# Optimization experiments

Measured on AMD Instinct MI355X. Metric: run time of the kernel, lower is better.

Reference implementation:

```python
import jax, jax.numpy as jnp
import numpy as np

JITTER = 0.05  # posterior-covariance jitter (constructor arg `jitter`)
TWO_PI = 2.0 * np.pi


def _local_k(x1, x2, ls, std):
    # 1-D RBF kernel: x1 (A,), x2 (B,) -> (A, B)
    d2 = jnp.square(x1[:, None] - x2[None, :])
    return (std * std) * jnp.exp(-0.5 * d2 / (ls * ls))


def setup_inputs() -> dict:
    key = jax.random.key(0)
    ks = jax.random.split(key, 8)
    N, D, M = 3072, 4, 512
    X = jax.random.normal(ks[0], (N, D), dtype=jnp.float32)
    y = jax.random.normal(ks[1], (N, 1), dtype=jnp.float32)
    X_bar = jax.random.normal(ks[2], (M, D), dtype=jnp.float32)
    # learned parameters (moderate positive values so fp32 Choleskys are stable)
    local_gp_ls = 1.0 + 0.1 * jax.random.normal(ks[3], (D,), dtype=jnp.float32)
    local_gp_std = 0.5 + 0.05 * jax.random.normal(ks[4], (D,), dtype=jnp.float32)
    local_gp_noise_std = 0.3 * jnp.ones((D,), dtype=jnp.float32)
    local_ls = 0.3 + 0.5 * jax.random.uniform(ks[5], (M, D), dtype=jnp.float32)
    global_gp_std = jnp.array([0.7], dtype=jnp.float32)
    global_gp_noise_std = jnp.array([0.5], dtype=jnp.float32)
    return {
        "X": X, "y": y, "X_bar": X_bar,
        "local_gp_ls": local_gp_ls, "local_gp_std": local_gp_std,
        "local_gp_noise_std": local_gp_noise_std, "local_ls": local_ls,
        "global_gp_std": global_gp_std, "global_gp_noise_std": global_gp_noise_std,
    }


def reference(X, y, X_bar, local_gp_ls, local_gp_std, local_gp_noise_std,
              local_ls, global_gp_std, global_gp_noise_std):
    # NSGP.nlml() in training mode.
    N, D = X.shape
    M = X_bar.shape[0]
    dtype = X.dtype
    eyeM = jnp.eye(M, dtype=dtype)
    eyeN = jnp.eye(N, dtype=dtype)
    log_lbar = jnp.log(jnp.abs(local_ls))  # (M, D)

    def per_dim(xb, xd, ls, std, noise, loglb):
        # local GP over inducing points for one input dimension
        k = _local_k(xb, xb, ls, std) + (noise * noise) * eyeM  # (M, M)
        c = jnp.linalg.cholesky(k)
        alpha = jax.scipy.linalg.cho_solve((c, True), loglb[:, None])  # (M, 1)
        kstar = _local_k(xd, xb, ls, std)  # (N, M)
        l = jnp.exp(kstar @ alpha)[:, 0]   # (N,) predicted lengthscales
        kss = _local_k(xd, xd, ls, std)    # (N, N)
        v = jax.scipy.linalg.cho_solve((c, True), kstar.T)  # (M, N)
        kpost = kss - kstar @ v + JITTER * eyeN             # posterior cov
        pc = jnp.linalg.cholesky(kpost)
        Bd = jnp.sum(jnp.log(jnp.diagonal(pc)))
        return l, Bd

    # batch the per-dimension local-GP work across the D input dims
    l_dn, B_d = jax.vmap(per_dim, in_axes=(1, 1, 0, 0, 0, 1))(
        X_bar, X, local_gp_ls, local_gp_std, local_gp_noise_std, log_lbar)
    l = l_dn.T  # (N, D)

    # nonstationary global kernel (Gibbs kernel)
    l1 = l[:, None, :]                    # (N, 1, D)
    l2 = l[None, :, :]                    # (1, N, D)
    lsq = l1 * l1 + l2 * l2               # (N, N, D)
    suffix = jnp.prod(jnp.sqrt(2.0 * l1 * l2 / lsq), axis=2)  # (N, N)
    d2 = jnp.square(X[:, None, :] - X[None, :, :])            # (N, N, D)
    gvar = global_gp_std[0] * global_gp_std[0]
    K = gvar * suffix * jnp.exp(-jnp.sum(d2 / lsq, axis=2))
    K = K + (global_gp_noise_std[0] ** 2) * eyeN

    L = jnp.linalg.cholesky(K)
    alpha = jax.scipy.linalg.cho_solve((L, True), y)  # (N, 1)
    log2pi = jnp.log(jnp.asarray(TWO_PI, dtype))
    A = 0.5 * ((y.T @ alpha)[0, 0]
               + jnp.sum(jnp.log(jnp.diagonal(L)))
               + N * log2pi)
    B = jnp.sum(B_d) + 0.5 * (M * D * log2pi)
    return A + B
```

## Files before the change

### kernel.cpp

```cpp
#include <hip/hip_runtime.h>
#include <math.h>

#define N_   3072
#define D_   4
#define M_   512
#define NPAD 3200
#define NB   128
#define PW   32
#define NBLK (NPAD/NB)
#define MBLK (M_/NB)
#define JITTER_ 0.05f
#define CBORD 32768.0f

__global__ __launch_bounds__(256)
void k_potrf_inv(float* Abase, size_t aStride, int lda, int kblk,
                 float* TinvBase, size_t tStride, int doInv,
                 float* logsum, int slotBase, int limit) {
  __shared__ float LT[NB*NB];
  __shared__ float Wp[10*PW*PW];
  __shared__ float Tt[3*PW*PW];
  __shared__ float pivd[NB];
  const int tid = threadIdx.x;
  float* A = Abase + (size_t)blockIdx.z * aStride;
  const int j0 = kblk * NB;

  for (int t = tid; t < NB*NB; t += 256) {
    int r = t & 127, c = t >> 7;
    LT[c*NB + r] = (c <= r) ? A[(size_t)(j0 + r)*lda + (j0 + c)] : 0.f;
  }
  __syncthreads();

  #pragma unroll
  for (int p = 0; p < 4; ++p) {
    const int pc0 = p*PW, pc1 = pc0 + PW;
    for (int j = pc0; j < pc1; ++j) {
      float d = fmaxf(LT[j*NB + j], 1e-30f);
      if (tid == 0) pivd[j] = d;
      float rd = 1.0f / d;
      int w = pc1 - 1 - j;
      for (int t = tid; t < w*NB; t += 256) {
        int c = j + 1 + (t >> 7);
        int i = t & 127;
        if (i >= c)
          LT[c*NB + i] -= LT[j*NB + i] * LT[j*NB + c] * rd;
      }
      __syncthreads();
    }
    for (int t = tid; t < PW*NB; t += 256) {
      int jc = pc0 + (t >> 7);
      int i  = t & 127;
      float dd = pivd[jc];
      if (i > jc)       LT[jc*NB + i] *= rsqrtf(dd);
      else if (i == jc) LT[jc*NB + i] = sqrtf(dd);
    }
    __syncthreads();
    if (pc1 < NB) {
      const int rem = NB - pc1;
      for (int t = tid; t < rem*rem; t += 256) {
        int cc = t / rem, rr = t - cc*rem;
        int c = pc1 + cc, i = pc1 + rr;
        if (i >= c) {
          float s = 0.f;
          #pragma unroll
          for (int jj = 0; jj < PW; ++jj)
            s += LT[(pc0+jj)*NB + i] * LT[(pc0+jj)*NB + c];
          LT[c*NB + i] -= s;
        }
      }
      __syncthreads();
    }
  }

  for (int t = tid; t < NB*NB; t += 256) {
    int r = t & 127, c = t >> 7;
    if (c <= r) A[(size_t)(j0 + r)*lda + (j0 + c)] = LT[c*NB + r];
  }
  {
    float lg = 0.f;
    if (tid < NB) {
      int g = j0 + tid;
      if (g < limit) lg = 0.5f * logf(pivd[tid]);
    }
    for (int o = 32; o; o >>= 1) lg += __shfl_down(lg, o);
    int wv = tid >> 6;
    if ((tid & 63) == 0 && wv < 2)
      logsum[(slotBase + blockIdx.z*32 + kblk)*2 + wv] = lg;
  }

  if (!doInv) return;

  for (int t = tid; t < 4*1024; t += 256) {
    int I = t >> 10, e = t & 1023;
    int r = e >> 5, c = e & 31;
    Wp[(I*(I+1)/2 + I)*1024 + e] = (r == c) ? 1.f : 0.f;
  }
  __syncthreads();
  {
    int wI = tid >> 6;
    int lane = tid & 63;
    float* Rb = &Wp[(wI*(wI+1)/2 + wI)*1024];
    for (int j = 0; j < 32; ++j) {
      float dinv = 1.0f / LT[(wI*32+j)*NB + (wI*32+j)];
      for (int t = lane; t < 1024; t += 64) {
        int i = t >> 5, c = t & 31;
        if (i > j && c <= j)
          Rb[i*32 + c] -= LT[(wI*32+j)*NB + (wI*32+i)] * Rb[j*32 + c] * dinv;
      }
      __syncthreads();
    }
    for (int t = lane; t < 1024; t += 64) {
      int i = t >> 5, c = t & 31;
      if (c <= i) Rb[t] *= 1.0f / LT[(wI*32+i)*NB + (wI*32+i)];
    }
    __syncthreads();
  }
  #pragma unroll
  for (int dist = 1; dist < 4; ++dist) {
    const int nb = 4 - dist;
    for (int t = tid; t < nb*1024; t += 256) {
      int b = t >> 10, e = t & 1023;
      int r = e >> 5, c = e & 31;
      int J = b, I = b + dist;
      float s = 0.f;
      for (int K = J; K < I; ++K) {
        const float* Wkj = &Wp[(K*(K+1)/2 + J)*1024];
        #pragma unroll
        for (int k = 0; k < 32; ++k)
          s += LT[(K*32+k)*NB + (I*32+r)] * Wkj[k*32 + c];
      }
      Tt[b*1024 + e] = s;
    }
    __syncthreads();
    for (int t = tid; t < nb*1024; t += 256) {
      int b = t >> 10, e = t & 1023;
      int r = e >> 5, c = e & 31;
      int J = b, I = b + dist;
      const float* Wii = &Wp[(I*(I+1)/2 + I)*1024];
      float s = 0.f;
      #pragma unroll
      for (int k = 0; k < 32; ++k)
        s += Wii[r*32 + k] * Tt[b*1024 + k*32 + c];
      Wp[(I*(I+1)/2 + J)*1024 + e] = -s;
    }
    __syncthreads();
  }
  {
    float* Tinv = TinvBase + (size_t)blockIdx.z * tStride;
    for (int t = tid; t < NB*32; t += 256) {
      int i = t >> 5, c4 = (t & 31) * 4;
      int I = i >> 5, J = c4 >> 5;
      float4 v;
      if (J <= I) {
        const float* Wij = &Wp[(I*(I+1)/2 + J)*1024 + (i & 31)*32 + (c4 & 31)];
        v = *(const float4*)Wij;
      } else v = make_float4(0.f, 0.f, 0.f, 0.f);
      *(float4*)&Tinv[i*NB + c4] = v;
    }
  }
}

__global__ __launch_bounds__(256)
void k_trsm(float* Abase, size_t aStride, int lda, int kblk,
            const float* TinvBase, size_t tStride) {
  __shared__ float As[32*68];
  __shared__ float Ts[32*132];
  const int tid = threadIdx.x;
  float* A = Abase + (size_t)blockIdx.z * aStride;
  const float* Tinv = TinvBase + (size_t)blockIdx.z * tStride;
  const int k0 = kblk * NB;
  const int row0 = k0 + NB + blockIdx.x * 64;
  const int tx = tid & 15, ty = tid >> 4;
  float acc[4][8];
  #pragma unroll
  for (int i = 0; i < 4; ++i)
    #pragma unroll
    for (int u = 0; u < 8; ++u) acc[i][u] = 0.f;
  for (int ks = 0; ks < NB; ks += 32) {
    for (int t = tid; t < 64*8; t += 256) {
      int r = t >> 3, q = t & 7;
      float4 v = *(const float4*)&A[(size_t)(row0 + r)*lda + k0 + ks + q*4];
      As[(q*4+0)*68 + r] = v.x; As[(q*4+1)*68 + r] = v.y;
      As[(q*4+2)*68 + r] = v.z; As[(q*4+3)*68 + r] = v.w;
    }
    for (int t = tid; t < 128*8; t += 256) {
      int c = t >> 3, q = t & 7;
      float4 v = *(const float4*)&Tinv[c*NB + ks + q*4];
      Ts[(q*4+0)*132 + c] = v.x; Ts[(q*4+1)*132 + c] = v.y;
      Ts[(q*4+2)*132 + c] = v.z; Ts[(q*4+3)*132 + c] = v.w;
    }
    __syncthreads();
    #pragma unroll
    for (int kk = 0; kk < 32; ++kk) {
      float a[4], b[8];
      *(float4*)a      = *(const float4*)&As[kk*68 + ty*4];
      *(float4*)&b[0]  = *(const float4*)&Ts[kk*132 + tx*8];
      *(float4*)&b[4]  = *(const float4*)&Ts[kk*132 + tx*8 + 4];
      #pragma unroll
      for (int i = 0; i < 4; ++i)
        #pragma unroll
        for (int u = 0; u < 8; ++u) acc[i][u] += a[i]*b[u];
    }
    __syncthreads();
  }
  #pragma unroll
  for (int i = 0; i < 4; ++i) {
    int r = row0 + ty*4 + i;
    *(float4*)&A[(size_t)r*lda + k0 + tx*8]     = make_float4(acc[i][0],acc[i][1],acc[i][2],acc[i][3]);
    *(float4*)&A[(size_t)r*lda + k0 + tx*8 + 4] = make_float4(acc[i][4],acc[i][5],acc[i][6],acc[i][7]);
  }
}

__global__ __launch_bounds__(256)
void k_syrk(float* Abase, size_t aStride, int lda, int kblk) {
  if (blockIdx.y > blockIdx.x) return;
  __shared__ float As[32*68];
  __shared__ float Bs[32*68];
  const int tid = threadIdx.x;
  float* A = Abase + (size_t)blockIdx.z * aStride;
  const int k0 = kblk * NB;
  const int row0 = k0 + NB + blockIdx.x * 64;
  const int col0 = k0 + NB + blockIdx.y * 64;
  const int tx = tid & 15, ty = tid >> 4;
  float acc[4][4];
  #pragma unroll
  for (int i=0;i<4;++i) { acc[i][0]=0.f;acc[i][1]=0.f;acc[i][2]=0.f;acc[i][3]=0.f; }
  for (int ks = 0; ks < NB; ks += 32) {
    for (int t = tid; t < 64*8; t += 256) {
      int r = t >> 3, q = t & 7;
      float4 v = *(const float4*)&A[(size_t)(row0 + r)*lda + k0 + ks + q*4];
      As[(q*4+0)*68 + r] = v.x; As[(q*4+1)*68 + r] = v.y;
      As[(q*4+2)*68 + r] = v.z; As[(q*4+3)*68 + r] = v.w;
      float4 w = *(const float4*)&A[(size_t)(col0 + r)*lda + k0 + ks + q*4];
      Bs[(q*4+0)*68 + r] = w.x; Bs[(q*4+1)*68 + r] = w.y;
      Bs[(q*4+2)*68 + r] = w.z; Bs[(q*4+3)*68 + r] = w.w;
    }
    __syncthreads();
    #pragma unroll
    for (int kk = 0; kk < 32; ++kk) {
      float a[4], b[4];
      *(float4*)a = *(const float4*)&As[kk*68 + ty*4];
      *(float4*)b = *(const float4*)&Bs[kk*68 + tx*4];
      #pragma unroll
      for (int i=0;i<4;++i)
        #pragma unroll
        for (int u=0;u<4;++u) acc[i][u] += a[i]*b[u];
    }
    __syncthreads();
  }
  #pragma unroll
  for (int i=0;i<4;++i) {
    size_t off = (size_t)(row0 + ty*4 + i)*lda + col0 + tx*4;
    float4 v = *(const float4*)&A[off];
    v.x -= acc[i][0]; v.y -= acc[i][1]; v.z -= acc[i][2]; v.w -= acc[i][3];
    *(float4*)&A[off] = v;
  }
}

__global__ __launch_bounds__(256)
void k_build_kb(const float* Xbar, const float* lsp, const float* stdp, const float* noisep,
                float* KbBase, size_t kbStride, int dimBase) {
  int z = blockIdx.z, d = dimBase + z;
  float* Kb = KbBase + (size_t)z*kbStride;
  int idx = blockIdx.x*256 + threadIdx.x;
  if (idx >= M_*M_) return;
  int i = idx >> 9, j = idx & 511;
  float ls = lsp[d], sd = stdp[d], nz = noisep[d];
  float df = Xbar[i*D_ + d] - Xbar[j*D_ + d];
  float v = sd*sd*expf(-0.5f*df*df/(ls*ls));
  if (i == j) v += nz*nz;
  Kb[idx] = v;
}

__global__ __launch_bounds__(256)
void k_build_kstar(const float* X, const float* Xbar, const float* lsp, const float* stdp,
                   float* KSBase, size_t ksStride, int dimBase) {
  int z = blockIdx.z, d = dimBase + z;
  float* KS = KSBase + (size_t)z*ksStride;
  int idx = blockIdx.x*256 + threadIdx.x;
  if (idx >= N_*M_) return;
  int i = idx >> 9, j = idx & 511;
  float ls = lsp[d], sd = stdp[d];
  float df = X[i*D_ + d] - Xbar[j*D_ + d];
  KS[idx] = sd*sd*expf(-0.5f*df*df/(ls*ls));
}

__global__ __launch_bounds__(256)
void k_csolve(float* CBase, size_t cStride, const float* KbBase, size_t kbStride,
              const float* TinvKbBase, size_t tkbStride, int J) {
  __shared__ float sm[12672];
  const int tid = threadIdx.x;
  float* C = CBase + (size_t)blockIdx.z*cStride;
  const float* L = KbBase + (size_t)blockIdx.z*kbStride;
  const float* Tinv = TinvKbBase + (size_t)blockIdx.z*tkbStride + (size_t)J*NB*NB;
  const int row0 = blockIdx.x*64;
  const int tx = tid & 15, ty = tid >> 4;
  float* As = sm; float* Ls = sm + 2176;
  float* Xs = sm; float* Ts = sm + 8448;
  float acc[4][8];
  #pragma unroll
  for (int i=0;i<4;++i) {
    const float* p = &C[(size_t)(row0+ty*4+i)*M_ + J*NB + tx*8];
    float4 v0 = *(const float4*)p, v1 = *(const float4*)(p+4);
    acc[i][0]=v0.x; acc[i][1]=v0.y; acc[i][2]=v0.z; acc[i][3]=v0.w;
    acc[i][4]=v1.x; acc[i][5]=v1.y; acc[i][6]=v1.z; acc[i][7]=v1.w;
  }
  for (int P = 0; P < J; ++P) {
    for (int ks = 0; ks < NB; ks += 32) {
      __syncthreads();
      for (int t = tid; t < 64*8; t += 256) {
        int r = t >> 3, q = t & 7;
        float4 v = *(const float4*)&C[(size_t)(row0+r)*M_ + P*NB + ks + q*4];
        As[(q*4+0)*68+r]=v.x; As[(q*4+1)*68+r]=v.y; As[(q*4+2)*68+r]=v.z; As[(q*4+3)*68+r]=v.w;
      }
      for (int t = tid; t < 128*8; t += 256) {
        int c = t >> 3, q = t & 7;
        float4 v = *(const float4*)&L[(size_t)(J*NB+c)*M_ + P*NB + ks + q*4];
        Ls[(q*4+0)*132+c]=v.x; Ls[(q*4+1)*132+c]=v.y; Ls[(q*4+2)*132+c]=v.z; Ls[(q*4+3)*132+c]=v.w;
      }
      __syncthreads();
      #pragma unroll
      for (int kk = 0; kk < 32; ++kk) {
        float a[4], b[8];
        *(float4*)a     = *(const float4*)&As[kk*68 + ty*4];
        *(float4*)&b[0] = *(const float4*)&Ls[kk*132 + tx*8];
        *(float4*)&b[4] = *(const float4*)&Ls[kk*132 + tx*8 + 4];
        #pragma unroll
        for (int i=0;i<4;++i)
          #pragma unroll
          for (int u=0;u<8;++u) acc[i][u] -= a[i]*b[u];
      }
    }
  }
  __syncthreads();
  #pragma unroll
  for (int i=0;i<4;++i)
    #pragma unroll
    for (int u=0;u<8;++u) Xs[(ty*4+i)*132 + tx*8+u] = acc[i][u];
  #pragma unroll
  for (int i=0;i<4;++i)
    #pragma unroll
    for (int u=0;u<8;++u) acc[i][u] = 0.f;
  for (int ms = 0; ms < NB; ms += 32) {
    for (int t = tid; t < 128*8; t += 256) {
      int c = t >> 3, q = t & 7;
      float4 v = *(const float4*)&Tinv[c*NB + ms + q*4];
      Ts[(q*4+0)*132+c]=v.x; Ts[(q*4+1)*132+c]=v.y; Ts[(q*4+2)*132+c]=v.z; Ts[(q*4+3)*132+c]=v.w;
    }
    __syncthreads();
    #pragma unroll
    for (int mm = 0; mm < 32; ++mm) {
      float a[4], b[8];
      a[0]=Xs[(ty*4+0)*132+ms+mm]; a[1]=Xs[(ty*4+1)*132+ms+mm];
      a[2]=Xs[(ty*4+2)*132+ms+mm]; a[3]=Xs[(ty*4+3)*132+ms+mm];
      *(float4*)&b[0] = *(const float4*)&Ts[mm*132 + tx*8];
      *(float4*)&b[4] = *(const float4*)&Ts[mm*132 + tx*8 + 4];
      #pragma unroll
      for (int i=0;i<4;++i)
        #pragma unroll
        for (int u=0;u<8;++u) acc[i][u] += a[i]*b[u];
    }
    __syncthreads();
  }
  #pragma unroll
  for (int i=0;i<4;++i) {
    float* p = &C[(size_t)(row0+ty*4+i)*M_ + J*NB + tx*8];
    *(float4*)p     = make_float4(acc[i][0],acc[i][1],acc[i][2],acc[i][3]);
    *(float4*)(p+4) = make_float4(acc[i][4],acc[i][5],acc[i][6],acc[i][7]);
  }
}

__global__ __launch_bounds__(256)
void k_fwdsub(const float* KbBase, size_t kbStride,
              const float* TkbBase, size_t tkbStride,
              const float* lls, float* wBase, size_t wStride, int dimBase) {
  __shared__ float w[M_];
  __shared__ float tv[NB];
  __shared__ float red[256];
  int z = blockIdx.z, d = dimBase + z;
  const float* L = KbBase + (size_t)z*kbStride;
  const float* Tk = TkbBase + (size_t)z*tkbStride;
  float* wout = wBase + (size_t)z*wStride;
  const int tid = threadIdx.x;
  for (int i = tid; i < M_; i += 256) w[i] = logf(fabsf(lls[i*D_ + d]));
  __syncthreads();
  const int r = tid >> 1, h = tid & 1;
  for (int J = 0; J < 4; ++J) {
    float s = 0.f;
    int half = (J*NB) >> 1;
    for (int k = h*half; k < (h+1)*half; k += 4) {
      float4 lv = *(const float4*)&L[(size_t)(J*NB + r)*M_ + k];
      s += lv.x*w[k] + lv.y*w[k+1] + lv.z*w[k+2] + lv.w*w[k+3];
    }
    red[tid] = s;
    __syncthreads();
    if (h == 0) tv[r] = w[J*NB + r] - red[2*r] - red[2*r+1];
    __syncthreads();
    const float* Ti = Tk + (size_t)J*NB*NB;
    s = 0.f;
    for (int k = h*64; k < h*64 + 64; k += 4) {
      float4 tw = *(const float4*)&Ti[r*NB + k];
      s += tw.x*tv[k] + tw.y*tv[k+1] + tw.z*tv[k+2] + tw.w*tv[k+3];
    }
    red[tid] = s;
    __syncthreads();
    if (h == 0) w[J*NB + r] = red[2*r] + red[2*r+1];
    __syncthreads();
  }
  for (int i = tid; i < M_; i += 256) wout[i] = w[i];
}

__global__ __launch_bounds__(256)
void k_gemv_l(const float* CBase, size_t cStride, const float* wBase, size_t wStride,
              float* lvec, int dimBase) {
  int z = blockIdx.z, d = dimBase + z;
  const float* C = CBase + (size_t)z*cStride;
  const float* w = wBase + (size_t)z*wStride;
  __shared__ float ws[M_];
  for (int i = threadIdx.x; i < M_; i += 256) ws[i] = w[i];
  __syncthreads();
  int wid = threadIdx.x >> 6, lane = threadIdx.x & 63;
  int row = blockIdx.x*4 + wid;
  if (row >= N_) return;
  float s = 0.f;
  const float* cr = &C[(size_t)row*M_];
  for (int k = lane; k < M_; k += 64) s += cr[k]*ws[k];
  for (int o = 32; o; o >>= 1) s += __shfl_down(s, o);
  if (lane == 0) lvec[row*D_ + d] = expf(s);
}

__global__ __launch_bounds__(256)
void k_kpost(const float* X, const float* lsp, const float* stdp,
             const float* CBase, size_t cStride,
             float* Abase, size_t aStride, int dimBase) {
  if (blockIdx.y > blockIdx.x) return;
  __shared__ float As[32*68];
  __shared__ float Bs[32*68];
  int z = blockIdx.z, d = dimBase + z;
  const float* C = CBase + (size_t)z*cStride;
  float* A = Abase + (size_t)z*aStride;
  const int row0 = blockIdx.x*64, col0 = blockIdx.y*64;
  const int tid = threadIdx.x, tx = tid & 15, ty = tid >> 4;
  float acc[4][4];
  #pragma unroll
  for (int i=0;i<4;++i) { acc[i][0]=0.f;acc[i][1]=0.f;acc[i][2]=0.f;acc[i][3]=0.f; }
  if (row0 < N_) {
    for (int ks = 0; ks < M_; ks += 32) {
      for (int t = tid; t < 64*8; t += 256) {
        int r = t >> 3, q = t & 7;
        float4 v = *(const float4*)&C[(size_t)(row0+r)*M_ + ks + q*4];
        As[(q*4+0)*68+r]=v.x; As[(q*4+1)*68+r]=v.y; As[(q*4+2)*68+r]=v.z; As[(q*4+3)*68+r]=v.w;
        float4 w2 = *(const float4*)&C[(size_t)(col0+r)*M_ + ks + q*4];
        Bs[(q*4+0)*68+r]=w2.x; Bs[(q*4+1)*68+r]=w2.y; Bs[(q*4+2)*68+r]=w2.z; Bs[(q*4+3)*68+r]=w2.w;
      }
      __syncthreads();
      #pragma unroll
      for (int kk=0; kk<32; ++kk) {
        float a[4], b[4];
        *(float4*)a = *(const float4*)&As[kk*68 + ty*4];
        *(float4*)b = *(const float4*)&Bs[kk*68 + tx*4];
        #pragma unroll
        for (int i=0;i<4;++i)
          #pragma unroll
          for (int u=0;u<4;++u) acc[i][u] += a[i]*b[u];
      }
      __syncthreads();
    }
  }
  float ls = lsp[d], sd = stdp[d];
  float inv2 = -0.5f/(ls*ls), s2 = sd*sd;
  #pragma unroll
  for (int i=0;i<4;++i) {
    int gi = row0 + ty*4 + i;
    float xi = (gi < N_) ? X[gi*D_ + d] : 0.f;
    #pragma unroll
    for (int u=0;u<4;++u) {
      int gj = col0 + tx*4 + u;
      float v;
      if (gi < N_ && gj < N_) {
        float df = xi - X[gj*D_ + d];
        v = s2*expf(inv2*df*df) - acc[i][u];
        if (gi == gj) v += JITTER_;
      } else {
        v = (gi == gj) ? 1.f : 0.f;
      }
      A[(size_t)gi*NPAD + gj] = v;
    }
  }
}

__global__ __launch_bounds__(256)
void k_kfinal(const float* X, const float* lvec, const float* y,
              const float* gstd, const float* gnoise, float* A) {
  int idx = blockIdx.x*256 + threadIdx.x;
  if (idx >= NPAD*NPAD) return;
  int gi = idx / NPAD, gj = idx - (idx/NPAD)*NPAD;
  float v;
  if (gi < N_ && gj < N_) {
    float gv = gstd[0]*gstd[0];
    float prod = 1.f, s = 0.f;
    #pragma unroll
    for (int d = 0; d < D_; ++d) {
      float l1 = lvec[gi*D_ + d], l2 = lvec[gj*D_ + d];
      float lsq = l1*l1 + l2*l2;
      prod *= 2.f*l1*l2/lsq;
      float df = X[gi*D_ + d] - X[gj*D_ + d];
      s += df*df/lsq;
    }
    v = gv * sqrtf(prod) * expf(-s);
    if (gi == gj) v += gnoise[0]*gnoise[0];
  } else if (gi == N_ && gj < N_) v = y[gj];
  else if (gj == N_ && gi < N_) v = y[gi];
  else if (gi == N_ && gj == N_) v = CBORD;
  else v = (gi == gj) ? 1.f : 0.f;
  A[idx] = v;
}

__global__ void k_finalize(const float* A, const float* logsum, float* out) {
  if (threadIdx.x != 0 || blockIdx.x != 0) return;
  float sumB = 0.f;
  for (int z = 0; z < 4; ++z)
    for (int k = 0; k < NBLK; ++k) {
      int slot = z*32 + k;
      sumB += logsum[slot*2] + logsum[slot*2+1];
    }
  float sumL = 0.f;
  for (int k = 0; k < NBLK; ++k) {
    int slot = 128 + k;
    sumL += logsum[slot*2] + logsum[slot*2+1];
  }
  float lb = A[(size_t)N_*NPAD + N_];
  float yKy = CBORD - lb*lb;
  const float LOG2PI = 1.8378770664093453f;
  float Aterm = 0.5f*(yKy + sumL + (float)N_*LOG2PI);
  float Bterm = sumB + 0.5f*(float)(M_*D_)*LOG2PI;
  out[0] = Aterm + Bterm;
}

extern "C" void kernel_launch(void* const* d_in, const int* in_sizes, int n_in,
                              void* d_out, int out_size, void* d_ws, size_t ws_size,
                              hipStream_t stream) {
  const float* X    = (const float*)d_in[0];
  const float* y    = (const float*)d_in[1];
  const float* Xbar = (const float*)d_in[2];
  const float* lgls = (const float*)d_in[3];
  const float* lgstd= (const float*)d_in[4];
  const float* lgnz = (const float*)d_in[5];
  const float* lls  = (const float*)d_in[6];
  const float* gstd = (const float*)d_in[7];
  const float* gnz  = (const float*)d_in[8];
  float* out = (float*)d_out;

  const size_t A_SZ   = (size_t)NPAD*NPAD;
  const size_t KS_SZ  = (size_t)N_*M_;
  const size_t KB_SZ  = (size_t)M_*M_;
  const size_t TKB_SZ = (size_t)4*NB*NB;
  const size_t TBG_SZ = (size_t)NB*NB;
  const size_t W_SZ   = (size_t)M_;
  const size_t LV_SZ  = (size_t)N_*D_;
  const size_t LOG_SZ = 1024;

  size_t need2 = (5*A_SZ + 4*(KS_SZ + KB_SZ + TKB_SZ + W_SZ) + 5*TBG_SZ
                  + LV_SZ + LOG_SZ + 1024);
  size_t per1  = A_SZ + KS_SZ + KB_SZ + TKB_SZ + TBG_SZ + W_SZ;
  size_t need1 = 4*per1 + LV_SZ + LOG_SZ + 256;

  if (ws_size >= need2 * sizeof(float)) {
    float* p = (float*)d_ws;
    float* A    = p; p += 5*A_SZ;
    float* KS   = p; p += 4*KS_SZ;
    float* Kb   = p; p += 4*KB_SZ;
    float* Tkb  = p; p += 4*TKB_SZ;
    float* Tbig = p; p += 5*TBG_SZ;
    float* wv   = p; p += 4*W_SZ;
    float* lv   = p; p += LV_SZ;
    float* lgs  = p; p += LOG_SZ;

    k_build_kb<<<dim3((M_*M_+255)/256,1,4),256,0,stream>>>(Xbar,lgls,lgstd,lgnz,Kb,KB_SZ,0);
    for (int k = 0; k < MBLK; ++k) {
      k_potrf_inv<<<dim3(1,1,4),256,0,stream>>>(Kb,KB_SZ,M_,k,Tkb+(size_t)k*NB*NB,TKB_SZ,1,lgs,192,0);
      if (k < MBLK-1) {
        int nt = (MBLK-1-k)*2;
        k_trsm<<<dim3(nt,1,4),256,0,stream>>>(Kb,KB_SZ,M_,k,Tkb+(size_t)k*NB*NB,TKB_SZ);
        k_syrk<<<dim3(nt,nt,4),256,0,stream>>>(Kb,KB_SZ,M_,k);
      }
    }
    k_fwdsub<<<dim3(1,1,4),256,0,stream>>>(Kb,KB_SZ,Tkb,TKB_SZ,lls,wv,W_SZ,0);
    k_build_kstar<<<dim3((N_*M_+255)/256,1,4),256,0,stream>>>(X,Xbar,lgls,lgstd,KS,KS_SZ,0);
    for (int J = 0; J < MBLK; ++J)
      k_csolve<<<dim3(N_/64,1,4),256,0,stream>>>(KS,KS_SZ,Kb,KB_SZ,Tkb,TKB_SZ,J);
    k_gemv_l<<<dim3(N_/4,1,4),256,0,stream>>>(KS,KS_SZ,wv,W_SZ,lv,0);
    k_kpost<<<dim3(NPAD/64,NPAD/64,4),256,0,stream>>>(X,lgls,lgstd,KS,KS_SZ,A,A_SZ,0);
    k_kfinal<<<dim3((NPAD*NPAD+255)/256,1,1),256,0,stream>>>(X,lv,y,gstd,gnz,A+4*A_SZ);
    for (int k = 0; k < NBLK; ++k) {
      k_potrf_inv<<<dim3(1,1,5),256,0,stream>>>(A,A_SZ,NPAD,k,Tbig,TBG_SZ,(k<NBLK-1)?1:0,lgs,0,N_);
      if (k < NBLK-1) {
        int nt = (NBLK-1-k)*2;
        k_trsm<<<dim3(nt,1,5),256,0,stream>>>(A,A_SZ,NPAD,k,Tbig,TBG_SZ);
        k_syrk<<<dim3(nt,nt,5),256,0,stream>>>(A,A_SZ,NPAD,k);
      }
    }
    k_finalize<<<1,64,0,stream>>>(A+4*A_SZ,lgs,out);
    return;
  }

  bool batched = ws_size >= need1 * sizeof(float);
  int nz = batched ? 4 : 1;

  float* p = (float*)d_ws;
  float* A    = p; p += (size_t)nz*A_SZ;
  float* KS   = p; p += (size_t)nz*KS_SZ;
  float* Kb   = p; p += (size_t)nz*KB_SZ;
  float* Tkb  = p; p += (size_t)nz*TKB_SZ;
  float* Tbig = p; p += (size_t)nz*TBG_SZ;
  float* wv   = p; p += (size_t)nz*W_SZ;
  float* lv   = p; p += LV_SZ;
  float* lgs  = p; p += LOG_SZ;

  int npass = batched ? 1 : 4;
  for (int pass = 0; pass < npass; ++pass) {
    int dimBase  = batched ? 0 : pass;
    int slotBase = batched ? 0 : pass*32;

    k_build_kb<<<dim3((M_*M_+255)/256,1,nz),256,0,stream>>>(Xbar,lgls,lgstd,lgnz,Kb,KB_SZ,dimBase);
    for (int k = 0; k < MBLK; ++k) {
      k_potrf_inv<<<dim3(1,1,nz),256,0,stream>>>(Kb,KB_SZ,M_,k,Tkb+(size_t)k*NB*NB,TKB_SZ,1,lgs,192+slotBase,0);
      if (k < MBLK-1) {
        int nt = (MBLK-1-k)*2;
        k_trsm<<<dim3(nt,1,nz),256,0,stream>>>(Kb,KB_SZ,M_,k,Tkb+(size_t)k*NB*NB,TKB_SZ);
        k_syrk<<<dim3(nt,nt,nz),256,0,stream>>>(Kb,KB_SZ,M_,k);
      }
    }
    k_fwdsub<<<dim3(1,1,nz),256,0,stream>>>(Kb,KB_SZ,Tkb,TKB_SZ,lls,wv,W_SZ,dimBase);
    k_build_kstar<<<dim3((N_*M_+255)/256,1,nz),256,0,stream>>>(X,Xbar,lgls,lgstd,KS,KS_SZ,dimBase);
    for (int J = 0; J < MBLK; ++J)
      k_csolve<<<dim3(N_/64,1,nz),256,0,stream>>>(KS,KS_SZ,Kb,KB_SZ,Tkb,TKB_SZ,J);
    k_gemv_l<<<dim3(N_/4,1,nz),256,0,stream>>>(KS,KS_SZ,wv,W_SZ,lv,dimBase);
    k_kpost<<<dim3(NPAD/64,NPAD/64,nz),256,0,stream>>>(X,lgls,lgstd,KS,KS_SZ,A,A_SZ,dimBase);
    for (int k = 0; k < NBLK; ++k) {
      k_potrf_inv<<<dim3(1,1,nz),256,0,stream>>>(A,A_SZ,NPAD,k,Tbig,TBG_SZ,(k<NBLK-1)?1:0,lgs,slotBase,N_);
      if (k < NBLK-1) {
        int nt = (NBLK-1-k)*2;
        k_trsm<<<dim3(nt,1,nz),256,0,stream>>>(A,A_SZ,NPAD,k,Tbig,TBG_SZ);
        k_syrk<<<dim3(nt,nt,nz),256,0,stream>>>(A,A_SZ,NPAD,k);
      }
    }
  }

  k_kfinal<<<dim3((NPAD*NPAD+255)/256,1,1),256,0,stream>>>(X,lv,y,gstd,gnz,A);
  for (int k = 0; k < NBLK; ++k) {
    k_potrf_inv<<<dim3(1,1,1),256,0,stream>>>(A,A_SZ,NPAD,k,Tbig,TBG_SZ,(k<NBLK-1)?1:0,lgs,128,N_);
    if (k < NBLK-1) {
      int nt = (NBLK-1-k)*2;
      k_trsm<<<dim3(nt,1,1),256,0,stream>>>(A,A_SZ,NPAD,k,Tbig,TBG_SZ);
      k_syrk<<<dim3(nt,nt,1),256,0,stream>>>(A,A_SZ,NPAD,k);
    }
  }
  k_finalize<<<1,64,0,stream>>>(A,lgs,out);
}
```

Before: 8.406 ms.

## Fuse blocked Cholesky into one persistent cooperative kernel with lookahead

Replaces the per-block potrf/trsm/syrk launch sequence with a single cooperative kernel of 256 workgroups that synchronises through grid.sync. In each step the next diagonal block is factored with its own panel update applied, while the other workgroups run the trailing SYRK update at the same time. This removes many small kernel launches and overlaps the serial diagonal factorization with the trailing update. In exchange it needs cooperative-launch support, puts a full grid barrier in every step, and gives the diagonal factorization and inverse to a single workgroup per matrix.

After: 9.608 ms. +14.3%, slower.

```diff
diff --git a/kernel.cpp b/kernel.cpp
--- a/kernel.cpp
+++ b/kernel.cpp
@@ -1,5 +1,8 @@
 #include <hip/hip_runtime.h>
+#include <hip/hip_cooperative_groups.h>
 #include <math.h>
+
+namespace cg = cooperative_groups;
 
 #define N_   3072
 #define D_   4
@@ -11,6 +14,305 @@
 #define MBLK (M_/NB)
 #define JITTER_ 0.05f
 #define CBORD 32768.0f
+#define CH_T  512
+#define CH_GRID 256
+
+
+__device__ void potrf_duty(float* A, int lda, int b, int presub,
+                           float* Tinv, float* logsum, int slot, int limit,
+                           float* LT, float* SM, float* pivd) {
+  const int tid = threadIdx.x;
+  const int j0 = b * NB;
+  for (int t = tid; t < NB*NB; t += CH_T) {
+    int r = t & 127, c = t >> 7;
+    LT[c*NB + r] = (c <= r) ? A[(size_t)(j0+r)*lda + (j0+c)] : 0.f;
+  }
+  if (presub) {
+    float* Pc = SM;
+    const int p0 = (b-1) * NB;
+    for (int cs = 0; cs < NB; cs += 32) {
+      __syncthreads();
+      for (int t = tid; t < 128*8; t += CH_T) {
+        int r = t >> 3, q = t & 7;
+        float4 v = *(const float4*)&A[(size_t)(j0+r)*lda + p0 + cs + q*4];
+        Pc[r*33 + q*4+0] = v.x; Pc[r*33 + q*4+1] = v.y;
+        Pc[r*33 + q*4+2] = v.z; Pc[r*33 + q*4+3] = v.w;
+      }
+      __syncthreads();
+      for (int t = tid; t < NB*NB; t += CH_T) {
+        int r = t & 127, c = t >> 7;
+        if (c <= r) {
+          float s = 0.f;
+          #pragma unroll
+          for (int kk = 0; kk < 32; ++kk) s += Pc[r*33+kk]*Pc[c*33+kk];
+          LT[c*NB + r] -= s;
+        }
+      }
+    }
+  }
+  __syncthreads();
+  #pragma unroll
+  for (int p = 0; p < 4; ++p) {
+    const int pc0 = p*PW, pc1 = pc0 + PW;
+    for (int j = pc0; j < pc1; ++j) {
+      float dd = fmaxf(LT[j*NB + j], 1e-30f);
+      if (tid == 0) pivd[j] = dd;
+      float rd = 1.0f / dd;
+      int wn = pc1 - 1 - j;
+      for (int t = tid; t < wn*NB; t += CH_T) {
+        int c = j + 1 + (t >> 7);
+        int i = t & 127;
+        if (i >= c) LT[c*NB + i] -= LT[j*NB + i] * LT[j*NB + c] * rd;
+      }
+      __syncthreads();
+    }
+    for (int t = tid; t < PW*NB; t += CH_T) {
+      int jc = pc0 + (t >> 7);
+      int i  = t & 127;
+      float dd = pivd[jc];
+      if (i > jc)       LT[jc*NB + i] *= rsqrtf(dd);
+      else if (i == jc) LT[jc*NB + i] = sqrtf(dd);
+    }
+    __syncthreads();
+    if (pc1 < NB) {
+      const int rem = NB - pc1;
+      for (int t = tid; t < rem*rem; t += CH_T) {
+        int cc = t / rem, rr = t - cc*rem;
+        int c = pc1 + cc, i = pc1 + rr;
+        if (i >= c) {
+          float s = 0.f;
+          #pragma unroll
+          for (int jj = 0; jj < PW; ++jj)
+            s += LT[(pc0+jj)*NB + i] * LT[(pc0+jj)*NB + c];
+          LT[c*NB + i] -= s;
+        }
+      }
+      __syncthreads();
+    }
+  }
+  for (int t = tid; t < NB*NB; t += CH_T) {
+    int r = t & 127, c = t >> 7;
+    if (c <= r) A[(size_t)(j0+r)*lda + (j0+c)] = LT[c*NB + r];
+  }
+  {
+    float lg = 0.f;
+    if (tid < NB) {
+      int g = j0 + tid;
+      if (g < limit) lg = 0.5f * logf(pivd[tid]);
+    }
+    for (int o = 32; o; o >>= 1) lg += __shfl_down(lg, o);
+    int wv = tid >> 6;
+    if ((tid & 63) == 0 && wv < 2) logsum[slot*2 + wv] = lg;
+  }
+  float* Wp = SM;
+  float* Tt = SM + 10240;
+  for (int t = tid; t < 4*1024; t += CH_T) {
+    int I = t >> 10, e = t & 1023;
+    int r = e >> 5, c = e & 31;
+    Wp[(I*(I+1)/2 + I)*1024 + e] = (r == c) ? 1.f : 0.f;
+  }
+  __syncthreads();
+  {
+    int wI = tid >> 7;
+    int lane = tid & 127;
+    float* Rb = &Wp[(wI*(wI+1)/2 + wI)*1024];
+    for (int j = 0; j < 32; ++j) {
+      float dinv = 1.0f / LT[(wI*32+j)*NB + (wI*32+j)];
+      for (int t = lane; t < 1024; t += 128) {
+        int i = t >> 5, c = t & 31;
+        if (i > j && c <= j)
+          Rb[i*32 + c] -= LT[(wI*32+j)*NB + (wI*32+i)] * Rb[j*32 + c] * dinv;
+      }
+      __syncthreads();
+    }
+    for (int t = lane; t < 1024; t += 128) {
+      int i = t >> 5, c = t & 31;
+      if (c <= i) Rb[i*32 + c] *= 1.0f / LT[(wI*32+i)*NB + (wI*32+i)];
+    }
+    __syncthreads();
+  }
+  #pragma unroll
+  for (int dist = 1; dist < 4; ++dist) {
+    const int nb = 4 - dist;
+    for (int t = tid; t < nb*1024; t += CH_T) {
+      int bb = t >> 10, e = t & 1023;
+      int r = e >> 5, c = e & 31;
+      int J = bb, I = bb + dist;
+      float s = 0.f;
+      for (int K = J; K < I; ++K) {
+        const float* Wkj = &Wp[(K*(K+1)/2 + J)*1024];
+        #pragma unroll
+        for (int k = 0; k < 32; ++k)
+          s += LT[(K*32+k)*NB + (I*32+r)] * Wkj[k*32 + c];
+      }
+      Tt[bb*1024 + e] = s;
+    }
+    __syncthreads();
+    for (int t = tid; t < nb*1024; t += CH_T) {
+      int bb = t >> 10, e = t & 1023;
+      int r = e >> 5, c = e & 31;
+      int J = bb, I = bb + dist;
+      const float* Wii = &Wp[(I*(I+1)/2 + I)*1024];
+      float s = 0.f;
+      #pragma unroll
+      for (int k = 0; k < 32; ++k)
+        s += Wii[r*32 + k] * Tt[bb*1024 + k*32 + c];
+      Wp[(I*(I+1)/2 + J)*1024 + e] = -s;
+    }
+    __syncthreads();
+  }
+  for (int t = tid; t < NB*32; t += CH_T) {
+    int i = t >> 5, c4 = (t & 31) * 4;
+    int I = i >> 5, J = c4 >> 5;
+    float4 v;
+    if (J <= I) {
+      const float* Wij = &Wp[(I*(I+1)/2 + J)*1024 + (i & 31)*32 + (c4 & 31)];
+      v = *(const float4*)Wij;
+    } else v = make_float4(0.f, 0.f, 0.f, 0.f);
+    *(float4*)&Tinv[i*NB + c4] = v;
+  }
+}
+
+__device__ void trsm_tile(float* A, int lda, int bi, int bk, const float* Tinv,
+                          float* As, float* Ts) {
+  const int tid = threadIdx.x;
+  const int tx = tid & 15, ty = tid >> 4;
+  const int r0 = bi*NB, k0 = bk*NB;
+  float acc[4][8];
+  #pragma unroll
+  for (int i = 0; i < 4; ++i)
+    #pragma unroll
+    for (int u = 0; u < 8; ++u) acc[i][u] = 0.f;
+  for (int ks = 0; ks < NB; ks += 32) {
+    __syncthreads();
+    for (int t = tid; t < 128*8; t += CH_T) {
+      int r = t >> 3, q = t & 7;
+      float4 v = *(const float4*)&A[(size_t)(r0+r)*lda + k0 + ks + q*4];
+      As[(q*4+0)*132+r]=v.x; As[(q*4+1)*132+r]=v.y;
+      As[(q*4+2)*132+r]=v.z; As[(q*4+3)*132+r]=v.w;
+      float4 w = *(const float4*)&Tinv[r*NB + ks + q*4];
+      Ts[(q*4+0)*132+r]=w.x; Ts[(q*4+1)*132+r]=w.y;
+      Ts[(q*4+2)*132+r]=w.z; Ts[(q*4+3)*132+r]=w.w;
+    }
+    __syncthreads();
+    #pragma unroll
+    for (int kk = 0; kk < 32; ++kk) {
+      float a[4], bb[8];
+      *(float4*)a      = *(const float4*)&As[kk*132 + ty*4];
+      *(float4*)&bb[0] = *(const float4*)&Ts[kk*132 + tx*8];
+      *(float4*)&bb[4] = *(const float4*)&Ts[kk*132 + tx*8 + 4];
+      #pragma unroll
+      for (int i = 0; i < 4; ++i)
+        #pragma unroll
+        for (int u = 0; u < 8; ++u) acc[i][u] += a[i]*bb[u];
+    }
+  }
+  #pragma unroll
+  for (int i = 0; i < 4; ++i) {
+    size_t off = (size_t)(r0 + ty*4 + i)*lda + k0 + tx*8;
+    *(float4*)&A[off]     = make_float4(acc[i][0],acc[i][1],acc[i][2],acc[i][3]);
+    *(float4*)&A[off + 4] = make_float4(acc[i][4],acc[i][5],acc[i][6],acc[i][7]);
+  }
+}
+
+__device__ void syrk_tile(float* A, int lda, int bi, int bj, int bk,
+                          float* As, float* Bs) {
+  const int tid = threadIdx.x;
+  const int tx = tid & 15, ty = tid >> 4;
+  const int r0 = bi*NB, c0 = bj*NB, k0 = bk*NB;
+  float acc[4][8];
+  #pragma unroll
+  for (int i = 0; i < 4; ++i)
+    #pragma unroll
+    for (int u = 0; u < 8; ++u) acc[i][u] = 0.f;
+  for (int ks = 0; ks < NB; ks += 32) {
+    __syncthreads();
+    for (int t = tid; t < 128*8; t += CH_T) {
+      int r = t >> 3, q = t & 7;
+      float4 v = *(const float4*)&A[(size_t)(r0+r)*lda + k0 + ks + q*4];
+      As[(q*4+0)*132+r]=v.x; As[(q*4+1)*132+r]=v.y;
+      As[(q*4+2)*132+r]=v.z; As[(q*4+3)*132+r]=v.w;
+      float4 w = *(const float4*)&A[(size_t)(c0+r)*lda + k0 + ks + q*4];
+      Bs[(q*4+0)*132+r]=w.x; Bs[(q*4+1)*132+r]=w.y;
+      Bs[(q*4+2)*132+r]=w.z; Bs[(q*4+3)*132+r]=w.w;
+    }
+    __syncthreads();
+    #pragma unroll
+    for (int kk = 0; kk < 32; ++kk) {
+      float a[4], bb[8];
+      *(float4*)a      = *(const float4*)&As[kk*132 + ty*4];
+      *(float4*)&bb[0] = *(const float4*)&Bs[kk*132 + tx*8];
+      *(float4*)&bb[4] = *(const float4*)&Bs[kk*132 + tx*8 + 4];
+      #pragma unroll
+      for (int i = 0; i < 4; ++i)
+        #pragma unroll
+        for (int u = 0; u < 8; ++u) acc[i][u] += a[i]*bb[u];
+    }
+  }
+  #pragma unroll
+  for (int i = 0; i < 4; ++i) {
+    size_t off = (size_t)(r0 + ty*4 + i)*lda + c0 + tx*8;
+    float4 v0 = *(const float4*)&A[off];
+    float4 v1 = *(const float4*)&A[off + 4];
+    v0.x -= acc[i][0]; v0.y -= acc[i][1]; v0.z -= acc[i][2]; v0.w -= acc[i][3];
+    v1.x -= acc[i][4]; v1.y -= acc[i][5]; v1.z -= acc[i][6]; v1.w -= acc[i][7];
+    *(float4*)&A[off]     = v0;
+    *(float4*)&A[off + 4] = v1;
+  }
+}
+
+__global__ __launch_bounds__(CH_T, 1)
+void k_chol_fused(float* Abase, size_t aStride, int lda, int nblk, int nmat,
+                  float* TinvBase, size_t tStrideZ, size_t tStrideK,
+                  float* logsum, int slotBase, int limit) {
+  __shared__ __align__(16) float LT[NB*NB];
+  __shared__ __align__(16) float SM[13312];
+  __shared__ float pivd[NB];
+  cg::grid_group grid = cg::this_grid();
+  const int wg  = blockIdx.x;
+  const int nwg = gridDim.x;
+
+  if (wg < nmat) {
+    potrf_duty(Abase + (size_t)wg*aStride, lda, 0, 0,
+               TinvBase + (size_t)wg*tStrideZ, logsum, slotBase + wg*32, limit,
+               LT, SM, pivd);
+  }
+  __threadfence();
+  grid.sync();
+
+  for (int k = 0; k <= nblk-2; ++k) {
+    const int m = nblk - 1 - k;
+    for (int g = wg; g < nmat*m; g += nwg) {
+      int z = g % nmat, ii = g / nmat;
+      trsm_tile(Abase + (size_t)z*aStride, lda, k+1+ii, k,
+                TinvBase + (size_t)z*tStrideZ + (size_t)k*tStrideK,
+                SM, SM + 4224);
+    }
+    __threadfence();
+    grid.sync();
+    if (wg < nmat) {
+      potrf_duty(Abase + (size_t)wg*aStride, lda, k+1, 1,
+                 TinvBase + (size_t)wg*tStrideZ + (size_t)(k+1)*tStrideK,
+                 logsum, slotBase + wg*32 + (k+1), limit, LT, SM, pivd);
+    } else {
+      int Ttri = m*(m+1)/2;
+      int nwork = nmat*(Ttri - 1);
+      int w = wg - nmat, nworkers = nwg - nmat;
+      for (int g = w; g < nwork; g += nworkers) {
+        int z = g / (Ttri - 1);
+        int idx = 1 + g % (Ttri - 1);
+        int iP = (int)((sqrtf(8.f*(float)idx + 1.f) - 1.f)*0.5f);
+        while ((iP+1)*(iP+2)/2 <= idx) ++iP;
+        while (iP*(iP+1)/2 > idx) --iP;
+        int jP = idx - iP*(iP+1)/2;
+        syrk_tile(Abase + (size_t)z*aStride, lda, k+1+iP, k+1+jP, k,
+                  SM, SM + 4224);
+      }
+    }
+    __threadfence();
+    grid.sync();
+  }
+}
 
 __global__ __launch_bounds__(256)
 void k_potrf_inv(float* Abase, size_t aStride, int lda, int kblk,
@@ -23,13 +325,11 @@
   const int tid = threadIdx.x;
   float* A = Abase + (size_t)blockIdx.z * aStride;
   const int j0 = kblk * NB;
-
   for (int t = tid; t < NB*NB; t += 256) {
     int r = t & 127, c = t >> 7;
     LT[c*NB + r] = (c <= r) ? A[(size_t)(j0 + r)*lda + (j0 + c)] : 0.f;
   }
   __syncthreads();
-
   #pragma unroll
   for (int p = 0; p < 4; ++p) {
     const int pc0 = p*PW, pc1 = pc0 + PW;
@@ -41,8 +341,7 @@
       for (int t = tid; t < w*NB; t += 256) {
         int c = j + 1 + (t >> 7);
         int i = t & 127;
-        if (i >= c)
-          LT[c*NB + i] -= LT[j*NB + i] * LT[j*NB + c] * rd;
+        if (i >= c) LT[c*NB + i] -= LT[j*NB + i] * LT[j*NB + c] * rd;
       }
       __syncthreads();
     }
@@ -70,7 +369,6 @@
       __syncthreads();
     }
   }
-
   for (int t = tid; t < NB*NB; t += 256) {
     int r = t & 127, c = t >> 7;
     if (c <= r) A[(size_t)(j0 + r)*lda + (j0 + c)] = LT[c*NB + r];
@@ -86,9 +384,7 @@
     if ((tid & 63) == 0 && wv < 2)
       logsum[(slotBase + blockIdx.z*32 + kblk)*2 + wv] = lg;
   }
-
   if (!doInv) return;
-
   for (int t = tid; t < 4*1024; t += 256) {
     int I = t >> 10, e = t & 1023;
     int r = e >> 5, c = e & 31;
@@ -564,6 +860,52 @@
   size_t per1  = A_SZ + KS_SZ + KB_SZ + TKB_SZ + TBG_SZ + W_SZ;
   size_t need1 = 4*per1 + LV_SZ + LOG_SZ + 256;
 
+  int coop = 0;
+  {
+    int dev = 0;
+    hipGetDevice(&dev);
+    hipDeviceGetAttribute(&coop, hipDeviceAttributeCooperativeLaunch, dev);
+  }
+
+  if (coop && ws_size >= need2 * sizeof(float)) {
+    float* p = (float*)d_ws;
+    float* A    = p; p += 5*A_SZ;
+    float* KS   = p; p += 4*KS_SZ;
+    float* Kb   = p; p += 4*KB_SZ;
+    float* Tkb  = p; p += 4*TKB_SZ;
+    float* Tbig = p; p += 5*TBG_SZ;
+    float* wv   = p; p += 4*W_SZ;
+    float* lv   = p; p += LV_SZ;
+    float* lgs  = p; p += LOG_SZ;
+
+    k_build_kb<<<dim3((M_*M_+255)/256,1,4),256,0,stream>>>(Xbar,lgls,lgstd,lgnz,Kb,KB_SZ,0);
+    {
+      float* Aa = Kb; size_t aS = KB_SZ; int lda_ = M_; int nblk_ = MBLK; int nmat_ = 4;
+      float* Tb = Tkb; size_t tz = TKB_SZ; size_t tk = (size_t)NB*NB;
+      float* lg_ = lgs; int sb = 192; int lim = 0;
+      void* args[] = {&Aa,&aS,&lda_,&nblk_,&nmat_,&Tb,&tz,&tk,&lg_,&sb,&lim};
+      hipLaunchCooperativeKernel((const void*)k_chol_fused, dim3(CH_GRID), dim3(CH_T),
+                                 args, 0, stream);
+    }
+    k_fwdsub<<<dim3(1,1,4),256,0,stream>>>(Kb,KB_SZ,Tkb,TKB_SZ,lls,wv,W_SZ,0);
+    k_build_kstar<<<dim3((N_*M_+255)/256,1,4),256,0,stream>>>(X,Xbar,lgls,lgstd,KS,KS_SZ,0);
+    for (int J = 0; J < MBLK; ++J)
+      k_csolve<<<dim3(N_/64,1,4),256,0,stream>>>(KS,KS_SZ,Kb,KB_SZ,Tkb,TKB_SZ,J);
+    k_gemv_l<<<dim3(N_/4,1,4),256,0,stream>>>(KS,KS_SZ,wv,W_SZ,lv,0);
+    k_kpost<<<dim3(NPAD/64,NPAD/64,4),256,0,stream>>>(X,lgls,lgstd,KS,KS_SZ,A,A_SZ,0);
+    k_kfinal<<<dim3((NPAD*NPAD+255)/256,1,1),256,0,stream>>>(X,lv,y,gstd,gnz,A+4*A_SZ);
+    {
+      float* Aa = A; size_t aS = A_SZ; int lda_ = NPAD; int nblk_ = NBLK; int nmat_ = 5;
+      float* Tb = Tbig; size_t tz = TBG_SZ; size_t tk = 0;
+      float* lg_ = lgs; int sb = 0; int lim = N_;
+      void* args[] = {&Aa,&aS,&lda_,&nblk_,&nmat_,&Tb,&tz,&tk,&lg_,&sb,&lim};
+      hipLaunchCooperativeKernel((const void*)k_chol_fused, dim3(CH_GRID), dim3(CH_T),
+                                 args, 0, stream);
+    }
+    k_finalize<<<1,64,0,stream>>>(A+4*A_SZ,lgs,out);
+    return;
+  }
+
   if (ws_size >= need2 * sizeof(float)) {
     float* p = (float*)d_ws;
     float* A    = p; p += 5*A_SZ;
@@ -605,7 +947,6 @@
 
   bool batched = ws_size >= need1 * sizeof(float);
   int nz = batched ? 4 : 1;
-
   float* p = (float*)d_ws;
   float* A    = p; p += (size_t)nz*A_SZ;
   float* KS   = p; p += (size_t)nz*KS_SZ;
@@ -620,7 +961,6 @@
   for (int pass = 0; pass < npass; ++pass) {
     int dimBase  = batched ? 0 : pass;
     int slotBase = batched ? 0 : pass*32;
-
     k_build_kb<<<dim3((M_*M_+255)/256,1,nz),256,0,stream>>>(Xbar,lgls,lgstd,lgnz,Kb,KB_SZ,dimBase);
     for (int k = 0; k < MBLK; ++k) {
       k_potrf_inv<<<dim3(1,1,nz),256,0,stream>>>(Kb,KB_SZ,M_,k,Tkb+(size_t)k*NB*NB,TKB_SZ,1,lgs,192+slotBase,0);
@@ -645,7 +985,6 @@
       }
     }
   }
-
   k_kfinal<<<dim3((NPAD*NPAD+255)/256,1,1),256,0,stream>>>(X,lv,y,gstd,gnz,A);
   for (int k = 0; k < NBLK; ++k) {
     k_potrf_inv<<<dim3(1,1,1),256,0,stream>>>(A,A_SZ,NPAD,k,Tbig,TBG_SZ,(k<NBLK-1)?1:0,lgs,128,N_);
```
